# Performance work log

Measured on AMD Instinct MI355X. Metric: run time of the kernel, lower is better.

The kernel has to match this reference:

```python
import jax, jax.numpy as jnp
import numpy as np

B, N, F_IN, F_OUT = 8, 2048, 256, 128
ALPHA = 0.2
NEG_BIG = -9000000000000000.0


def setup_inputs() -> dict:
    key = jax.random.key(0)
    k1, k2, k3, k4 = jax.random.split(key, 4)
    X = jax.random.normal(k1, (B, N, F_IN), dtype=jnp.float32)
    # sparse-ish binary adjacency with self loops (faithful: module only needs 0/1 mask)
    A = (jax.random.uniform(k2, (B, N, N)) < 0.05).astype(jnp.float32)
    eye = jnp.eye(N, dtype=jnp.float32)[None]
    A = jnp.maximum(A, eye)
    # xavier_uniform-style init
    limW = float(np.sqrt(6.0 / (F_IN + F_OUT)))
    W = jax.random.uniform(k3, (F_IN, F_OUT), minval=-limW, maxval=limW, dtype=jnp.float32)
    lima = float(np.sqrt(6.0 / (2 * F_OUT + 1)))
    a = jax.random.uniform(k4, (2 * F_OUT, 1), minval=-lima, maxval=lima, dtype=jnp.float32)
    return {"X": X, "A": A, "W": W, "a": a}


def reference(X, A, W, a):
    # Wh: [B, N, F_OUT]
    Wh = jnp.einsum('bni,io->bno', X, W)
    # split a into source/dest halves: e_ij = leaky_relu(a1.Wh_i + a2.Wh_j)
    # (algebraically identical to cat([Wh_i, Wh_j]) @ a, avoids BxNxNx2F tensor)
    a1 = a[:F_OUT, 0]   # [F_OUT]
    a2 = a[F_OUT:, 0]   # [F_OUT]
    s1 = Wh @ a1        # [B, N]
    s2 = Wh @ a2        # [B, N]
    e = jax.nn.leaky_relu(s1[:, :, None] + s2[:, None, :], negative_slope=ALPHA)  # [B,N,N]
    e = e + NEG_BIG * (1.0 - A)
    attention = jax.nn.softmax(e, axis=-1)
    h_prime = jnp.einsum('bmn,bno->bmo', attention, Wh)
    return h_prime
```

## Files before the change

### kernel.cpp

```cpp
#include <hip/hip_runtime.h>
#include <math.h>

#define B_DIM 8
#define N_DIM 2048
#define F_IN 256
#define F_OUT 128
#define ALPHA 0.2f
#define KPAD 136
#define NT_TILE 128
#define TILES 16
#define BSTR 136

typedef __attribute__((ext_vector_type(8))) short short8;
typedef __attribute__((ext_vector_type(4))) float floatx4;

static __device__ __forceinline__ unsigned short f2bf(float f) {
    unsigned u = __float_as_uint(f);
    u += 0x7fff + ((u >> 16) & 1);
    return (unsigned short)(u >> 16);
}
static __device__ __forceinline__ float bf2f(unsigned short s) {
    return __uint_as_float((unsigned)s << 16);
}
static __device__ __forceinline__ unsigned fmap(float f) {
    int b = __float_as_int(f);
    return (unsigned)(b ^ ((b >> 31) | 0x80000000));
}
static __device__ __forceinline__ float funmap(unsigned u) {
    return __uint_as_float((u & 0x80000000u) ? (int)(u ^ 0x80000000u) : ~(int)u);
}

__global__ __launch_bounds__(256) void gemm_xw(const float* __restrict__ X,
                                               const float* __restrict__ W,
                                               const float* __restrict__ avec,
                                               unsigned short* __restrict__ WhT,
                                               float* __restrict__ s1,
                                               float* __restrict__ s2,
                                               unsigned* __restrict__ s2max_u) {
    __shared__ unsigned short Wt[F_OUT][KPAD];
    const int t = threadIdx.x;
    const int lane = t & 63, wave = t >> 6;
    const int m = lane & 15, q = lane >> 4;
    const int row0 = blockIdx.x * 64 + wave * 16;

    floatx4 acc[8];
#pragma unroll
    for (int nt = 0; nt < 8; nt++) acc[nt] = (floatx4){0.f, 0.f, 0.f, 0.f};

    const int n0 = (t & 31) * 4;
    const int kb = t >> 5;

    for (int half = 0; half < 2; half++) {
        const float* Wp = W + (size_t)(half * 128 + kb) * F_OUT + n0;
#pragma unroll
        for (int i = 0; i < 16; i++) {
            float4 w = *(const float4*)(Wp + (size_t)i * 8 * F_OUT);
            int kk = kb + i * 8;
            Wt[n0 + 0][kk] = f2bf(w.x);
            Wt[n0 + 1][kk] = f2bf(w.y);
            Wt[n0 + 2][kk] = f2bf(w.z);
            Wt[n0 + 3][kk] = f2bf(w.w);
        }
        __syncthreads();

        const float* xrow = X + (size_t)(row0 + m) * F_IN + half * 128 + q * 8;
        float4 xr[8];
#pragma unroll
        for (int kt = 0; kt < 4; kt++) {
            xr[2 * kt] = *(const float4*)(xrow + kt * 32);
            xr[2 * kt + 1] = *(const float4*)(xrow + kt * 32 + 4);
        }
#pragma unroll
        for (int kt = 0; kt < 4; kt++) {
            union { unsigned short u[8]; short8 v; } af;
            float tmp[8] = {xr[2 * kt].x, xr[2 * kt].y, xr[2 * kt].z, xr[2 * kt].w,
                            xr[2 * kt + 1].x, xr[2 * kt + 1].y, xr[2 * kt + 1].z, xr[2 * kt + 1].w};
#pragma unroll
            for (int j = 0; j < 8; j++) af.u[j] = f2bf(tmp[j]);
#pragma unroll
            for (int nt = 0; nt < 8; nt++) {
                short8 bv = *(const short8*)&Wt[nt * 16 + m][kt * 32 + q * 8];
                acc[nt] = __builtin_amdgcn_mfma_f32_16x16x32_bf16(af.v, bv, acc[nt], 0, 0, 0);
            }
        }
        __syncthreads();
    }

    const int b = row0 >> 11;
    unsigned short* WTb = WhT + (size_t)b * F_OUT * N_DIM;
#pragma unroll
    for (int nt = 0; nt < 8; nt++) {
#pragma unroll
        for (int r = 0; r < 4; r++) {
            int nloc = (row0 & 2047) + q * 4 + r;
            WTb[(size_t)(nt * 16 + m) * N_DIM + nloc] = f2bf(acc[nt][r]);
        }
    }
    float a1v[8], a2v[8];
#pragma unroll
    for (int nt = 0; nt < 8; nt++) {
        a1v[nt] = avec[nt * 16 + m];
        a2v[nt] = avec[F_OUT + nt * 16 + m];
    }
    float wmax = -1e30f;
#pragma unroll
    for (int r = 0; r < 4; r++) {
        float v1 = 0.f, v2 = 0.f;
#pragma unroll
        for (int nt = 0; nt < 8; nt++) {
            v1 = fmaf(acc[nt][r], a1v[nt], v1);
            v2 = fmaf(acc[nt][r], a2v[nt], v2);
        }
#pragma unroll
        for (int mk = 8; mk >= 1; mk >>= 1) {
            v1 += __shfl_xor(v1, mk, 64);
            v2 += __shfl_xor(v2, mk, 64);
        }
        if (m == 0) {
            int row = row0 + q * 4 + r;
            s1[row] = v1;
            s2[row] = v2;
        }
        wmax = fmaxf(wmax, v2);
    }
    wmax = fmaxf(wmax, __shfl_xor(wmax, 16, 64));
    wmax = fmaxf(wmax, __shfl_xor(wmax, 32, 64));
    if (lane == 0) atomicMax(&s2max_u[b], fmap(wmax));
}

__global__ __launch_bounds__(256) void attn_mm(const float* __restrict__ A,
                                               const unsigned short* __restrict__ WhT,
                                               const float* __restrict__ s1,
                                               const float* __restrict__ s2,
                                               const unsigned* __restrict__ s2max_u,
                                               float* __restrict__ out) {
    __shared__ unsigned short Bs[2][F_OUT][BSTR];
    __shared__ float s2l[N_DIM];

    const int t = threadIdx.x;
    const int lane = t & 63, wave = t >> 6;
    const int m = lane & 15, q = lane >> 4;
    const int row0 = blockIdx.x * 64;
    const int b = row0 >> 11;
    const unsigned short* WTb = WhT + (size_t)b * F_OUT * N_DIM;

    {
        const float4* sg = (const float4*)(s2 + (size_t)b * N_DIM);
        *(float4*)&s2l[t * 8] = sg[t * 2];
        *(float4*)&s2l[t * 8 + 4] = sg[t * 2 + 1];
    }

    const int myrow = row0 + wave * 16 + m;
    const float s1m = s1[myrow];
    const float s2mx = funmap(s2max_u[b]);
    const float xs = s1m + s2mx;
    const float shift = fmaxf(xs, ALPHA * xs);
    const float* Arow = A + (size_t)myrow * N_DIM;

    const int g = t & 15, colb = t >> 4;

    float4 a_cur[8], a_nxt[8];
#pragma unroll
    for (int c = 0; c < 4; c++) {
        a_cur[2 * c] = *(const float4*)(Arow + c * 32 + q * 8);
        a_cur[2 * c + 1] = *(const float4*)(Arow + c * 32 + q * 8 + 4);
    }
    uint4 sreg[8];
#pragma unroll
    for (int i = 0; i < 8; i++)
        sreg[i] = *(const uint4*)(WTb + (size_t)(colb + i * 16) * N_DIM + g * 8);
#pragma unroll
    for (int i = 0; i < 8; i++)
        *(uint4*)&Bs[0][colb + i * 16][g * 8] = sreg[i];

    floatx4 acc[8];
#pragma unroll
    for (int nt = 0; nt < 8; nt++) acc[nt] = (floatx4){0.f, 0.f, 0.f, 0.f};
    float lsum = 0.f;

    __syncthreads();

    for (int tl = 0; tl < TILES; ++tl) {
        const int cur = tl & 1, nxt = cur ^ 1;
        if (tl + 1 < TILES) {
            const float* An = Arow + (tl + 1) * NT_TILE;
#pragma unroll
            for (int c = 0; c < 4; c++) {
                a_nxt[2 * c] = *(const float4*)(An + c * 32 + q * 8);
                a_nxt[2 * c + 1] = *(const float4*)(An + c * 32 + q * 8 + 4);
            }
            const unsigned short* Wn = WTb + (size_t)(tl + 1) * NT_TILE + g * 8;
#pragma unroll
            for (int i = 0; i < 8; i++)
                sreg[i] = *(const uint4*)(Wn + (size_t)(colb + i * 16) * N_DIM);
        }
        short8 pf[4];
#pragma unroll
        for (int c = 0; c < 4; c++) {
            float4 sa = *(const float4*)&s2l[tl * NT_TILE + c * 32 + q * 8];
            float4 sb = *(const float4*)&s2l[tl * NT_TILE + c * 32 + q * 8 + 4];
            float aa[8] = {a_cur[2 * c].x, a_cur[2 * c].y, a_cur[2 * c].z, a_cur[2 * c].w,
                           a_cur[2 * c + 1].x, a_cur[2 * c + 1].y, a_cur[2 * c + 1].z, a_cur[2 * c + 1].w};
            float zz[8] = {sa.x, sa.y, sa.z, sa.w, sb.x, sb.y, sb.z, sb.w};
            union { unsigned short u[8]; short8 v; } pu;
#pragma unroll
            for (int j = 0; j < 8; j++) {
                float x = s1m + zz[j];
                float e = fmaxf(x, ALPHA * x);
                float p = aa[j] * __expf(e - shift);
                unsigned short pb = f2bf(p);
                pu.u[j] = pb;
                lsum += bf2f(pb);
            }
            pf[c] = pu.v;
        }
#pragma unroll
        for (int c = 0; c < 4; c++)
#pragma unroll
            for (int nt = 0; nt < 8; nt++) {
                short8 bv = *(const short8*)&Bs[cur][nt * 16 + m][c * 32 + q * 8];
                acc[nt] = __builtin_amdgcn_mfma_f32_16x16x32_bf16(pf[c], bv, acc[nt], 0, 0, 0);
            }
        if (tl + 1 < TILES) {
#pragma unroll
            for (int i = 0; i < 8; i++)
                *(uint4*)&Bs[nxt][colb + i * 16][g * 8] = sreg[i];
#pragma unroll
            for (int i = 0; i < 8; i++) a_cur[i] = a_nxt[i];
        }
        __syncthreads();
    }

    lsum += __shfl_xor(lsum, 16, 64);
    lsum += __shfl_xor(lsum, 32, 64);
    const float inv = 1.f / lsum;
#pragma unroll
    for (int r = 0; r < 4; r++) {
        float invr = __shfl(inv, q * 4 + r, 64);
        float* orow = out + (size_t)(row0 + wave * 16 + q * 4 + r) * F_OUT + m;
#pragma unroll
        for (int nt = 0; nt < 8; nt++) orow[nt * 16] = acc[nt][r] * invr;
    }
}

extern "C" void kernel_launch(void* const* d_in, const int* in_sizes, int n_in,
                              void* d_out, int out_size, void* d_ws, size_t ws_size,
                              hipStream_t stream) {
    const float* X = (const float*)d_in[0];
    const float* A = (const float*)d_in[1];
    const float* W = (const float*)d_in[2];
    const float* avec = (const float*)d_in[3];
    float* out = (float*)d_out;

    unsigned short* WhT = (unsigned short*)d_ws;
    float* s1 = (float*)((char*)d_ws + (size_t)B_DIM * F_OUT * N_DIM * 2);
    float* s2 = s1 + B_DIM * N_DIM;
    unsigned* s2max_u = (unsigned*)(s2 + B_DIM * N_DIM);

    hipMemsetAsync(s2max_u, 0, B_DIM * sizeof(unsigned), stream);
    gemm_xw<<<B_DIM * N_DIM / 64, 256, 0, stream>>>(X, W, avec, WhT, s1, s2, s2max_u);
    attn_mm<<<B_DIM * N_DIM / 64, 256, 0, stream>>>(A, WhT, s1, s2, s2max_u, out);
}
```

Before: 261.0 us.

## Split attention key dimension across blocks with partial sums and epilogue reduce

The attention-times-Wh kernel now splits the 2048-key dimension into 4 chunks, launching 4x more blocks that each write unnormalized partial accumulators and row sums to workspace. A new epilogue kernel then reduces the partials and normalizes. The WhT tile is stored in shared memory in an MFMA-fragment-ordered layout, which drops padding and bank-conflict concerns, and s2 is read straight from global memory instead of being staged. Software double-buffering is removed in favour of more resident blocks. The cost is extra partial-sum traffic of about 32 MB and one more kernel launch.

```diff
diff --git a/kernel.cpp b/kernel.cpp
--- a/kernel.cpp
+++ b/kernel.cpp
@@ -7,9 +7,9 @@
 #define F_OUT 128
 #define ALPHA 0.2f
 #define KPAD 136
-#define NT_TILE 128
-#define TILES 16
-#define BSTR 136
+#define NSPLIT 4
+#define TPB 4
+#define PS ((size_t)B_DIM * N_DIM * F_OUT)
 
 typedef __attribute__((ext_vector_type(8))) short short8;
 typedef __attribute__((ext_vector_type(4))) float floatx4;
@@ -133,75 +133,61 @@
                                                const float* __restrict__ s1,
                                                const float* __restrict__ s2,
                                                const unsigned* __restrict__ s2max_u,
-                                               float* __restrict__ out) {
-    __shared__ unsigned short Bs[2][F_OUT][BSTR];
-    __shared__ float s2l[N_DIM];
+                                               float* __restrict__ pacc,
+                                               float* __restrict__ plsum) {
+    __shared__ unsigned short Bs[2048 * 8];
 
     const int t = threadIdx.x;
     const int lane = t & 63, wave = t >> 6;
     const int m = lane & 15, q = lane >> 4;
-    const int row0 = blockIdx.x * 64;
+    const int ns = blockIdx.x >> 8;
+    const int rg = blockIdx.x & 255;
+    const int row0 = rg * 64;
     const int b = row0 >> 11;
+    const int nbase = ns * 512;
+
     const unsigned short* WTb = WhT + (size_t)b * F_OUT * N_DIM;
-
-    {
-        const float4* sg = (const float4*)(s2 + (size_t)b * N_DIM);
-        *(float4*)&s2l[t * 8] = sg[t * 2];
-        *(float4*)&s2l[t * 8 + 4] = sg[t * 2 + 1];
-    }
-
     const int myrow = row0 + wave * 16 + m;
     const float s1m = s1[myrow];
     const float s2mx = funmap(s2max_u[b]);
     const float xs = s1m + s2mx;
     const float shift = fmaxf(xs, ALPHA * xs);
     const float* Arow = A + (size_t)myrow * N_DIM;
-
-    const int g = t & 15, colb = t >> 4;
-
-    float4 a_cur[8], a_nxt[8];
-#pragma unroll
-    for (int c = 0; c < 4; c++) {
-        a_cur[2 * c] = *(const float4*)(Arow + c * 32 + q * 8);
-        a_cur[2 * c + 1] = *(const float4*)(Arow + c * 32 + q * 8 + 4);
-    }
-    uint4 sreg[8];
-#pragma unroll
-    for (int i = 0; i < 8; i++)
-        sreg[i] = *(const uint4*)(WTb + (size_t)(colb + i * 16) * N_DIM + g * 8);
-#pragma unroll
-    for (int i = 0; i < 8; i++)
-        *(uint4*)&Bs[0][colb + i * 16][g * 8] = sreg[i];
+    const float* s2b = s2 + (size_t)b * N_DIM;
+
+    const int c_s0 = t >> 6;
 
     floatx4 acc[8];
 #pragma unroll
     for (int nt = 0; nt < 8; nt++) acc[nt] = (floatx4){0.f, 0.f, 0.f, 0.f};
     float lsum = 0.f;
 
-    __syncthreads();
-
-    for (int tl = 0; tl < TILES; ++tl) {
-        const int cur = tl & 1, nxt = cur ^ 1;
-        if (tl + 1 < TILES) {
-            const float* An = Arow + (tl + 1) * NT_TILE;
-#pragma unroll
-            for (int c = 0; c < 4; c++) {
-                a_nxt[2 * c] = *(const float4*)(An + c * 32 + q * 8);
-                a_nxt[2 * c + 1] = *(const float4*)(An + c * 32 + q * 8 + 4);
-            }
-            const unsigned short* Wn = WTb + (size_t)(tl + 1) * NT_TILE + g * 8;
-#pragma unroll
-            for (int i = 0; i < 8; i++)
-                sreg[i] = *(const uint4*)(Wn + (size_t)(colb + i * 16) * N_DIM);
-        }
+    for (int tl = 0; tl < TPB; tl++) {
+        const int noff = nbase + tl * 128;
+
+        float4 areg[8], zreg[8];
+#pragma unroll
+        for (int c = 0; c < 4; c++) {
+            areg[2 * c] = *(const float4*)(Arow + noff + c * 32 + q * 8);
+            areg[2 * c + 1] = *(const float4*)(Arow + noff + c * 32 + q * 8 + 4);
+            zreg[2 * c] = *(const float4*)(s2b + noff + c * 32 + q * 8);
+            zreg[2 * c + 1] = *(const float4*)(s2b + noff + c * 32 + q * 8 + 4);
+        }
+        uint4 sreg[8];
+#pragma unroll
+        for (int i = 0; i < 8; i++) {
+            int iw = i * 4 + c_s0;
+            int cs = iw & 3, nts = iw >> 2;
+            sreg[i] = *(const uint4*)(WTb + (size_t)(nts * 16 + m) * N_DIM + noff + cs * 32 + q * 8);
+        }
+
         short8 pf[4];
 #pragma unroll
         for (int c = 0; c < 4; c++) {
-            float4 sa = *(const float4*)&s2l[tl * NT_TILE + c * 32 + q * 8];
-            float4 sb = *(const float4*)&s2l[tl * NT_TILE + c * 32 + q * 8 + 4];
-            float aa[8] = {a_cur[2 * c].x, a_cur[2 * c].y, a_cur[2 * c].z, a_cur[2 * c].w,
-                           a_cur[2 * c + 1].x, a_cur[2 * c + 1].y, a_cur[2 * c + 1].z, a_cur[2 * c + 1].w};
-            float zz[8] = {sa.x, sa.y, sa.z, sa.w, sb.x, sb.y, sb.z, sb.w};
+            float aa[8] = {areg[2 * c].x, areg[2 * c].y, areg[2 * c].z, areg[2 * c].w,
+                           areg[2 * c + 1].x, areg[2 * c + 1].y, areg[2 * c + 1].z, areg[2 * c + 1].w};
+            float zz[8] = {zreg[2 * c].x, zreg[2 * c].y, zreg[2 * c].z, zreg[2 * c].w,
+                           zreg[2 * c + 1].x, zreg[2 * c + 1].y, zreg[2 * c + 1].z, zreg[2 * c + 1].w};
             union { unsigned short u[8]; short8 v; } pu;
 #pragma unroll
             for (int j = 0; j < 8; j++) {
@@ -214,33 +200,53 @@
             }
             pf[c] = pu.v;
         }
+
+#pragma unroll
+        for (int i = 0; i < 8; i++)
+            *(uint4*)&Bs[(size_t)(i * 256 + t) * 8] = sreg[i];
+        __syncthreads();
+
 #pragma unroll
         for (int c = 0; c < 4; c++)
 #pragma unroll
             for (int nt = 0; nt < 8; nt++) {
-                short8 bv = *(const short8*)&Bs[cur][nt * 16 + m][c * 32 + q * 8];
+                short8 bv = *(const short8*)&Bs[(size_t)((nt * 4 + c) * 64 + lane) * 8];
                 acc[nt] = __builtin_amdgcn_mfma_f32_16x16x32_bf16(pf[c], bv, acc[nt], 0, 0, 0);
             }
-        if (tl + 1 < TILES) {
-#pragma unroll
-            for (int i = 0; i < 8; i++)
-                *(uint4*)&Bs[nxt][colb + i * 16][g * 8] = sreg[i];
-#pragma unroll
-            for (int i = 0; i < 8; i++) a_cur[i] = a_nxt[i];
-        }
         __syncthreads();
     }
 
     lsum += __shfl_xor(lsum, 16, 64);
     lsum += __shfl_xor(lsum, 32, 64);
-    const float inv = 1.f / lsum;
+    if (q == 0) plsum[(size_t)ns * (B_DIM * N_DIM) + row0 + wave * 16 + m] = lsum;
+
+    float* pa = pacc + (size_t)ns * PS;
 #pragma unroll
     for (int r = 0; r < 4; r++) {
-        float invr = __shfl(inv, q * 4 + r, 64);
-        float* orow = out + (size_t)(row0 + wave * 16 + q * 4 + r) * F_OUT + m;
-#pragma unroll
-        for (int nt = 0; nt < 8; nt++) orow[nt * 16] = acc[nt][r] * invr;
-    }
+        float* prow = pa + (size_t)(row0 + wave * 16 + q * 4 + r) * F_OUT + m;
+#pragma unroll
+        for (int nt = 0; nt < 8; nt++) prow[nt * 16] = acc[nt][r];
+    }
+}
+
+__global__ __launch_bounds__(256) void epi(const float* __restrict__ pacc,
+                                           const float* __restrict__ plsum,
+                                           float* __restrict__ out) {
+    const int t = threadIdx.x;
+    const int row = blockIdx.x * 8 + (t >> 5);
+    const int c0 = (t & 31) * 4;
+    float l = 0.f;
+#pragma unroll
+    for (int ns = 0; ns < NSPLIT; ns++) l += plsum[(size_t)ns * (B_DIM * N_DIM) + row];
+    float4 v = make_float4(0.f, 0.f, 0.f, 0.f);
+#pragma unroll
+    for (int ns = 0; ns < NSPLIT; ns++) {
+        float4 p = *(const float4*)(pacc + (size_t)ns * PS + (size_t)row * F_OUT + c0);
+        v.x += p.x; v.y += p.y; v.z += p.z; v.w += p.w;
+    }
+    const float inv = 1.f / l;
+    v.x *= inv; v.y *= inv; v.z *= inv; v.w *= inv;
+    *(float4*)(out + (size_t)row * F_OUT + c0) = v;
 }
 
 extern "C" void kernel_launch(void* const* d_in, const int* in_sizes, int n_in,
@@ -252,12 +258,16 @@
     const float* avec = (const float*)d_in[3];
     float* out = (float*)d_out;
 
-    unsigned short* WhT = (unsigned short*)d_ws;
-    float* s1 = (float*)((char*)d_ws + (size_t)B_DIM * F_OUT * N_DIM * 2);
-    float* s2 = s1 + B_DIM * N_DIM;
-    unsigned* s2max_u = (unsigned*)(s2 + B_DIM * N_DIM);
+    char* ws = (char*)d_ws;
+    unsigned short* WhT = (unsigned short*)ws;            ws += PS * 2;
+    float* s1 = (float*)ws;                               ws += B_DIM * N_DIM * 4;
+    float* s2 = (float*)ws;                               ws += B_DIM * N_DIM * 4;
+    unsigned* s2max_u = (unsigned*)ws;                    ws += 256;
+    float* pacc = (float*)ws;                             ws += PS * NSPLIT * 4;
+    float* plsum = (float*)ws;
 
     hipMemsetAsync(s2max_u, 0, B_DIM * sizeof(unsigned), stream);
     gemm_xw<<<B_DIM * N_DIM / 64, 256, 0, stream>>>(X, W, avec, WhT, s1, s2, s2max_u);
-    attn_mm<<<B_DIM * N_DIM / 64, 256, 0, stream>>>(A, WhT, s1, s2, s2max_u, out);
-}
+    attn_mm<<<256 * NSPLIT, 256, 0, stream>>>(A, WhT, s1, s2, s2max_u, pacc, plsum);
+    epi<<<B_DIM * N_DIM / 8, 256, 0, stream>>>(pacc, plsum, out);
+}
```

Measured after the change: 258.9 us. No clear change (-0.8%).
